# Performance work log

Measured on AMD Instinct MI355X. Metric: run time of the kernel, lower is better.

Reference implementation:

```python
import jax, jax.numpy as jnp
from jax import lax
import numpy as np

EPS = 1e-5
DN = ('NCHW', 'OIHW', 'NCHW')


def conv_s2(x, w):
    # Conv2d k=4 s=2 p=1, no bias
    return lax.conv_general_dilated(x, w, (2, 2), [(1, 1), (1, 1)], dimension_numbers=DN)


def deconv_s2(x, w):
    # ConvTranspose2d k=4 s=2 p=1; torch weight layout (in, out, kH, kW)
    w_ = jnp.flip(w, (2, 3)).transpose(1, 0, 2, 3)  # -> (out, in, kH, kW)
    return lax.conv_general_dilated(x, w_, (1, 1), [(2, 2), (2, 2)],
                                    lhs_dilation=(2, 2), dimension_numbers=DN)


def bn_train(x, gamma, beta):
    # BatchNorm2d in training mode: batch stats over (N, H, W), biased variance
    m = jnp.mean(x, axis=(0, 2, 3), keepdims=True)
    v = jnp.var(x, axis=(0, 2, 3), keepdims=True)
    g = gamma.reshape(1, -1, 1, 1)
    b = beta.reshape(1, -1, 1, 1)
    return (x - m) * jax.lax.rsqrt(v + EPS) * g + b


def lrelu(x):
    return jnp.where(x >= 0, x, 0.2 * x)


def setup_inputs() -> dict:
    key = jax.random.key(0)
    ks = jax.random.split(key, 32)
    nef = 64
    d = {}
    d['x'] = jax.random.normal(ks[0], (256, 3, 64, 64), dtype=jnp.float32)
    # encoder conv weights (O, I, 4, 4), init N(0, 0.02)
    d['w1'] = 0.02 * jax.random.normal(ks[1], (nef, 3, 4, 4), jnp.float32)
    d['w2'] = 0.02 * jax.random.normal(ks[2], (nef * 2, nef, 4, 4), jnp.float32)
    d['w3'] = 0.02 * jax.random.normal(ks[3], (nef * 4, nef * 2, 4, 4), jnp.float32)
    d['w4'] = 0.02 * jax.random.normal(ks[4], (nef * 8, nef * 4, 4, 4), jnp.float32)
    # bn params: weight ~ N(1, 0.02), bias = 0
    for i, c in enumerate([nef, nef * 2, nef * 4, nef * 8]):
        d[f'g{i+1}'] = 1.0 + 0.02 * jax.random.normal(ks[5 + i], (c,), jnp.float32)
        d[f'b{i+1}'] = jnp.zeros((c,), jnp.float32)
    # 512 channel-wise Linear(16,16): torch default init U(-1/4, 1/4)
    bound = 1.0 / 4.0
    d['cw_w'] = jax.random.uniform(ks[9], (512, 16, 16), jnp.float32, -bound, bound)
    d['cw_b'] = jax.random.uniform(ks[10], (512, 16), jnp.float32, -bound, bound)
    # decoder deconv weights in torch layout (in, out, 4, 4)
    d['dw1'] = 0.02 * jax.random.normal(ks[11], (nef * 8, nef * 4, 4, 4), jnp.float32)
    d['dw2'] = 0.02 * jax.random.normal(ks[12], (nef * 4, nef * 2, 4, 4), jnp.float32)
    d['dw3'] = 0.02 * jax.random.normal(ks[13], (nef * 2, nef, 4, 4), jnp.float32)
    d['dw4'] = 0.02 * jax.random.normal(ks[14], (nef, 3, 4, 4), jnp.float32)
    for i, c in enumerate([nef * 4, nef * 2, nef]):
        d[f'dg{i+1}'] = 1.0 + 0.02 * jax.random.normal(ks[15 + i], (c,), jnp.float32)
        d[f'db{i+1}'] = jnp.zeros((c,), jnp.float32)
    return d


def reference(x, w1, w2, w3, w4, g1, b1, g2, b2, g3, b3, g4, b4,
              cw_w, cw_b, dw1, dw2, dw3, dw4, dg1, db1, dg2, db2, dg3, db3):
    h = lrelu(bn_train(conv_s2(x, w1), g1, b1))
    h = lrelu(bn_train(conv_s2(h, w2), g2, b2))
    h = lrelu(bn_train(conv_s2(h, w3), g3, b3))
    h = lrelu(bn_train(conv_s2(h, w4), g4, b4))  # (B, 512, 4, 4)
    B, C, H, W = h.shape
    flat = h.reshape(B, C, H * W)  # (B, 512, 16)
    # per-channel Linear: y[b,c,t] = sum_s flat[b,c,s] * cw_w[c,t,s] + cw_b[c,t]
    flat = jnp.einsum('bcs,cts->bct', flat, cw_w) + cw_b[None, :, :]
    h = flat.reshape(B, C, H, W)
    h = jax.nn.relu(bn_train(deconv_s2(h, dw1), dg1, db1))
    h = jax.nn.relu(bn_train(deconv_s2(h, dw2), dg2, db2))
    h = jax.nn.relu(bn_train(deconv_s2(h, dw3), dg3, db3))
    return jnp.tanh(deconv_s2(h, dw4))
```

## Files before the change

### kernel.cpp

```cpp
#include <hip/hip_runtime.h>
#include <math.h>

typedef _Float16 f16;
typedef __attribute__((ext_vector_type(8))) _Float16 f16x8;
typedef __attribute__((ext_vector_type(16))) float f32x16;

union U64x2 { unsigned long long u[2]; f16x8 v; };
union Q16   { uint4 q; unsigned long long u[2]; };

constexpr int ilog2c(int x) { return x <= 1 ? 0 : 1 + ilog2c(x >> 1); }

__device__ __forceinline__ float fast_tanh(float x) {
    float e = __expf(2.f * x);
    return (e - 1.f) / (e + 1.f);
}

__device__ __forceinline__ void barrier_no_vmdrain() {
    asm volatile("s_waitcnt lgkmcnt(0)" ::: "memory");
    __builtin_amdgcn_sched_barrier(0);
    __builtin_amdgcn_s_barrier();
    __builtin_amdgcn_sched_barrier(0);
}

template<int CIN,int IH,int IW,int OH,int OW,int COUT,int COB,int SPT,int KS,
         int CO_FR,bool DEC,bool PAIR>
__global__ __launch_bounds__(256,2) void mfma_conv(
    const f16* __restrict__ xin, const f16* __restrict__ wp,
    f16* __restrict__ out16, float* __restrict__ out32, size_t ps,
    float* __restrict__ psumF, float* __restrict__ psqF)
{
    constexpr int OHo  = DEC ? OH/2 : OH;
    constexpr int OWo  = DEC ? OW/2 : OW;
    constexpr int KTOT = CIN * (DEC ? 4 : 16);
    constexpr int CH   = (KTOT/64) / KS;
    constexpr int RPT  = CIN / 64;
    constexpr int RSH  = (RPT==1?0:RPT==2?1:RPT==4?2:3);
    constexpr int WSTR = CIN * 16;
    constexpr int TPR  = 256 / COB;
    constexpr int SPB  = OHo * OWo;
    constexpr int LSPB = ilog2c(SPB);
    constexpr int LOWo = ilog2c(OWo);

    static_assert(!PAIR || (RPT >= 2 && CH % 2 == 0), "PAIR needs RPT>=2");
    constexpr int CHU  = PAIR ? CH/2 : CH;
    constexpr int RW   = PAIR ? 32 : 16;
    constexpr int PM   = PAIR ? 15 : 7;
    constexpr int KKN  = PAIR ? 8 : 4;
    constexpr int XU4  = PAIR ? 16 : 8;
    constexpr int WSEG = (PAIR ? 128 : 64)/TPR;
    constexpr int WU4  = WSEG / 8;

    __shared__ unsigned long long Xs[SPT*RW];
    __shared__ unsigned long long Wls[COB*RW];

    const int t   = threadIdx.x;
    const int bx  = blockIdx.x;
    const int cob = blockIdx.y;
    const int bz  = blockIdx.z;
    const int par = DEC ? (bz & 3) : 0;
    const int ks  = DEC ? (bz >> 2) : bz;
    const int poh = par >> 1, pw = par & 1;

    const int gsp_s = bx*SPT + t;
    const int img_s = gsp_s >> LSPB;
    const int r_s   = gsp_s & (SPB-1);
    const int oy_s  = r_s >> LOWo;
    const int ox_s  = r_s & (OWo-1);

    const int wco   = t / TPR;
    const int wpart = t % TPR;
    const f16* wbase = wp + (size_t)(cob*COB + wco)*WSTR + wpart*WSEG;

    const int wave = t >> 6, lane = t & 63, half = lane >> 5, l31 = lane & 31;
    const int co_w = (wave >> 1) * (CO_FR*32);
    const int sp_w = (wave & 1) * 128;
    const int swz  = l31 & PM;

    f32x16 acc[CO_FR][4];
    #pragma unroll
    for (int i = 0; i < CO_FR; ++i)
        #pragma unroll
        for (int b = 0; b < 4; ++b)
            #pragma unroll
            for (int r = 0; r < 16; ++r) acc[i][b][r] = 0.f;

    uint4 xreg[XU4];
    uint4 wreg[WU4];

    auto issue = [&](int cc) {
        const int gc  = ks*CH + (PAIR ? 2*cc : cc);
        const int tap = gc >> RSH;
        const int ci0 = (gc & (RPT-1)) << 6;
        int kh, kw, ih, iw;
        if (DEC) {
            const int t2h = tap >> 1, t2w = tap & 1;
            kh = (1-poh) + 2*t2h; kw = (1-pw) + 2*t2w;
            ih = oy_s + poh - t2h; iw = ox_s + pw - t2w;
        } else {
            kh = tap >> 2; kw = tap & 3;
            ih = 2*oy_s - 1 + kh; iw = 2*ox_s - 1 + kw;
        }
        const int woff = (kh*4 + kw)*CIN + ci0;
        const uint4* wsrc = (const uint4*)(wbase + woff);
        #pragma unroll
        for (int j = 0; j < WU4; ++j) wreg[j] = wsrc[j];
        const bool ok = (unsigned)ih < (unsigned)IH && (unsigned)iw < (unsigned)IW;
        if (ok) {
            const uint4* xsrc = (const uint4*)
                (xin + ((size_t)(img_s*IH + ih)*IW + iw)*CIN + ci0);
            #pragma unroll
            for (int j = 0; j < XU4; ++j) xreg[j] = xsrc[j];
        } else {
            #pragma unroll
            for (int j = 0; j < XU4; ++j) xreg[j] = uint4{0u,0u,0u,0u};
        }
    };

    issue(0);

    for (int cc = 0; cc < CHU; ++cc) {
        if (cc) barrier_no_vmdrain();

        #pragma unroll
        for (int j = 0; j < WU4; ++j) {
            Q16 v; v.q = wreg[j];
            const int lp = wpart*WU4 + j;
            const int u0 = wco*RW + ((lp ^ (wco & PM)) << 1);
            Wls[u0]   = v.u[0];
            Wls[u0+1] = v.u[1];
        }
        {
            #pragma unroll
            for (int j = 0; j < XU4; ++j) {
                Q16 v; v.q = xreg[j];
                const int u0 = t*RW + ((j ^ (t & PM)) << 1);
                Xs[u0]   = v.u[0];
                Xs[u0+1] = v.u[1];
            }
        }

        if (cc + 1 < CHU) issue(cc + 1);

        asm volatile("s_waitcnt lgkmcnt(0)" ::: "memory");
        __builtin_amdgcn_sched_barrier(0);
        __builtin_amdgcn_s_barrier();
        __builtin_amdgcn_sched_barrier(0);

        #pragma unroll
        for (int kk = 0; kk < KKN; ++kk) {
            const int so = ((kk*2 + half) ^ swz) << 1;
            f16x8 wf[CO_FR], xf[4];
            #pragma unroll
            for (int i = 0; i < CO_FR; ++i) {
                U64x2 u; const int rw = (co_w + i*32 + l31)*RW + so;
                u.u[0] = Wls[rw]; u.u[1] = Wls[rw+1]; wf[i] = u.v;
            }
            #pragma unroll
            for (int b = 0; b < 4; ++b) {
                U64x2 u; const int rx = (sp_w + b*32 + l31)*RW + so;
                u.u[0] = Xs[rx]; u.u[1] = Xs[rx+1]; xf[b] = u.v;
            }
            #pragma unroll
            for (int i = 0; i < CO_FR; ++i)
                #pragma unroll
                for (int b = 0; b < 4; ++b)
                    acc[i][b] = __builtin_amdgcn_mfma_f32_32x32x16_f16(
                        xf[b], wf[i], acc[i][b], 0, 0, 0);
        }
    }

    #pragma unroll
    for (int b = 0; b < 4; ++b) {
        #pragma unroll
        for (int q = 0; q < 4; ++q) {
            #pragma unroll
            for (int r2 = 0; r2 < 4; ++r2) {
                const int sp_loc = sp_w + b*32 + q*8 + 4*half + r2;
                const int gsp    = bx*SPT + sp_loc;
                size_t base;
                if (DEC) {
                    const int img = gsp >> LSPB;
                    const int r   = gsp & (SPB-1);
                    const int oh  = 2*(r >> LOWo) + poh;
                    const int ow  = 2*(r & (OWo-1)) + pw;
                    base = ((size_t)(img*OH + oh)*OW + ow)*COUT + cob*COB;
                } else {
                    base = (size_t)gsp*COUT + cob*COB;
                }
                #pragma unroll
                for (int i = 0; i < CO_FR; ++i) {
                    const int co_l = co_w + i*32 + l31;
                    const float v  = acc[i][b][q*4 + r2];
                    if (KS == 1) out16[base + co_l] = (_Float16)v;
                    else         out32[(size_t)ks*ps + base + co_l] = v;
                }
            }
        }
    }

    if (KS == 1 && psumF != nullptr) {
        float sArr[CO_FR], qArr[CO_FR];
        #pragma unroll
        for (int i = 0; i < CO_FR; ++i) {
            float s = 0.f, q = 0.f;
            #pragma unroll
            for (int b = 0; b < 4; ++b)
                #pragma unroll
                for (int r = 0; r < 16; ++r) {
                    const float v = acc[i][b][r];
                    s += v; q += v * v;
                }
            s += __shfl_down(s, 32);
            q += __shfl_down(q, 32);
            sArr[i] = s; qArr[i] = q;
        }
        __syncthreads();
        float* LS = (float*)Xs;
        float* LQ = LS + 4*CO_FR*32;
        if (half == 0) {
            #pragma unroll
            for (int i = 0; i < CO_FR; ++i) {
                LS[(wave*CO_FR + i)*32 + l31] = sArr[i];
                LQ[(wave*CO_FR + i)*32 + l31] = qArr[i];
            }
        }
        __syncthreads();
        if (t < COB) {
            constexpr int KSH = (CO_FR == 1 ? 5 : 6);
            const int k  = t >> KSH;
            const int ii = (CO_FR == 1) ? 0 : ((t >> 5) & 1);
            const int l  = t & 31;
            const int i0 = ((2*k)  *CO_FR + ii)*32 + l;
            const int i1 = ((2*k+1)*CO_FR + ii)*32 + l;
            atomicAdd(psumF + cob*COB + t, LS[i0] + LS[i1]);
            atomicAdd(psqF  + cob*COB + t, LQ[i0] + LQ[i1]);
        }
    }
}

__global__ __launch_bounds__(256,2) void conv1_mfma(
    const f16* __restrict__ xp, const f16* __restrict__ wp,
    f16* __restrict__ out, float* __restrict__ psumF, float* __restrict__ psqF)
{
    __shared__ unsigned long long Xs[256*16];
    __shared__ unsigned long long Wls[64*16];
    const int t = threadIdx.x, bx = blockIdx.x;

    {
        const int r = t >> 2, part = t & 3;
        const uint4* src = (const uint4*)(wp + r*64 + part*16);
        Q16 v0; v0.q = src[0];
        Q16 v1; v1.q = src[1];
        const int a0 = r*16 + (((part*2)   ^ (r & 7)) << 1);
        const int a1 = r*16 + (((part*2+1) ^ (r & 7)) << 1);
        Wls[a0]   = v0.u[0]; Wls[a0+1] = v0.u[1];
        Wls[a1]   = v1.u[0]; Wls[a1+1] = v1.u[1];
    }
    {
        const int gsp = bx*256 + t;
        const int n = gsp >> 10, r = gsp & 1023;
        const int oy = r >> 5, ox = r & 31;
        const int ih0 = 2*oy - 1, iw0 = 2*ox - 1;
        #pragma unroll
        for (int tap = 0; tap < 16; ++tap) {
            const int ih = ih0 + (tap >> 2), iw = iw0 + (tap & 3);
            unsigned long long v = 0ull;
            if ((unsigned)ih < 64u && (unsigned)iw < 64u)
                v = *(const unsigned long long*)(xp + (((size_t)n*64 + ih)*64 + iw)*4);
            const int u = t*16 + (((tap >> 1) ^ (t & 7)) << 1) + (tap & 1);
            Xs[u] = v;
        }
    }
    __syncthreads();

    const int wave = t >> 6, lane = t & 63, half = lane >> 5, l31 = lane & 31;
    const int co_w = (wave >> 1) * 32;
    const int sp_w = (wave & 1) * 128;
    const int swz  = l31 & 7;

    f32x16 acc[4];
    #pragma unroll
    for (int b = 0; b < 4; ++b)
        #pragma unroll
        for (int r = 0; r < 16; ++r) acc[b][r] = 0.f;

    #pragma unroll
    for (int kk = 0; kk < 4; ++kk) {
        const int so = ((kk*2 + half) ^ swz) << 1;
        U64x2 uw; const int rw = (co_w + l31)*16 + so;
        uw.u[0] = Wls[rw]; uw.u[1] = Wls[rw+1];
        #pragma unroll
        for (int b = 0; b < 4; ++b) {
            U64x2 ux; const int rx = (sp_w + b*32 + l31)*16 + so;
            ux.u[0] = Xs[rx]; ux.u[1] = Xs[rx+1];
            acc[b] = __builtin_amdgcn_mfma_f32_32x32x16_f16(
                ux.v, uw.v, acc[b], 0, 0, 0);
        }
    }
    #pragma unroll
    for (int b = 0; b < 4; ++b)
        #pragma unroll
        for (int q = 0; q < 4; ++q)
            #pragma unroll
            for (int r2 = 0; r2 < 4; ++r2) {
                const int sp_loc = sp_w + b*32 + q*8 + 4*half + r2;
                out[(size_t)(bx*256 + sp_loc)*64 + co_w + l31] =
                    (_Float16)acc[b][q*4 + r2];
            }

    float s = 0.f, q = 0.f;
    #pragma unroll
    for (int b = 0; b < 4; ++b)
        #pragma unroll
        for (int r = 0; r < 16; ++r) {
            const float v = acc[b][r];
            s += v; q += v * v;
        }
    s += __shfl_down(s, 32);
    q += __shfl_down(q, 32);
    __syncthreads();
    {
        float* LS = (float*)Xs;
        float* LQ = LS + 128;
        if (half == 0) {
            LS[wave*32 + l31] = s;
            LQ[wave*32 + l31] = q;
        }
        __syncthreads();
        if (t < 64) {
            const int k = t >> 5, l = t & 31;
            atomicAdd(psumF + t, LS[(2*k)*32 + l] + LS[(2*k+1)*32 + l]);
            atomicAdd(psqF  + t, LQ[(2*k)*32 + l] + LQ[(2*k+1)*32 + l]);
        }
    }
}

__global__ __launch_bounds__(256,2) void deconv4_mfma(
    const f16* __restrict__ xin, const f16* __restrict__ wp,
    float* __restrict__ out)
{
    __shared__ unsigned long long Xs[256*16];
    __shared__ unsigned long long Wls[4][32*16];

    const int t   = threadIdx.x;
    const int bx  = blockIdx.x;

    const int gsp_s = bx*256 + t;
    const int img_s = gsp_s >> 10;
    const int r_s   = gsp_s & 1023;
    const int oy_s  = r_s >> 5;
    const int ox_s  = r_s & 31;

    const int wco   = t >> 3;
    const int wpart = t & 7;

    const int wave = t >> 6, lane = t & 63, half = lane >> 5, l31 = lane & 31;
    const int sp_w = wave * 64;
    const int swz  = l31 & 7;

    f32x16 acc[4][2];
    #pragma unroll
    for (int p = 0; p < 4; ++p)
        #pragma unroll
        for (int b = 0; b < 2; ++b)
            #pragma unroll
            for (int r = 0; r < 16; ++r) acc[p][b][r] = 0.f;

    uint4 xreg[8];

    auto issueX = [&](int oid) {
        const int dh = oid/3 - 1, dw = oid%3 - 1;
        const int ih = oy_s + dh, iw = ox_s + dw;
        const bool ok = (unsigned)ih < 32u && (unsigned)iw < 32u;
        if (ok) {
            const uint4* src = (const uint4*)
                (xin + ((size_t)(img_s*32 + ih)*32 + iw)*64);
            #pragma unroll
            for (int j = 0; j < 8; ++j) xreg[j] = src[j];
        } else {
            #pragma unroll
            for (int j = 0; j < 8; ++j) xreg[j] = uint4{0u,0u,0u,0u};
        }
    };

    issueX(0);

    #pragma unroll
    for (int oid = 0; oid < 9; ++oid) {
        const int dh = oid/3 - 1, dw = oid%3 - 1;
        const int nH = (dh == 0) ? 2 : 1;
        const int nW = (dw == 0) ? 2 : 1;

        if (oid) barrier_no_vmdrain();

        uint4 wregc[4];
        #pragma unroll
        for (int ch = 0; ch < 2; ++ch) {
            #pragma unroll
            for (int cw = 0; cw < 2; ++cw) {
                if (ch < nH && cw < nW) {
                    const int poh_ = (dh == -1) ? 0 : (dh == 1) ? 1 : ch;
                    const int pw_  = (dw == -1) ? 0 : (dw == 1) ? 1 : cw;
                    const int kh   = (1 - poh_) + 2*(poh_ - dh);
                    const int kw   = (1 - pw_)  + 2*(pw_  - dw);
                    wregc[ch*2+cw] = *(const uint4*)
                        (wp + wco*1024 + (kh*4 + kw)*64 + wpart*8);
                }
            }
        }

        #pragma unroll
        for (int j = 0; j < 8; ++j) {
            Q16 v; v.q = xreg[j];
            const int u0 = t*16 + ((j ^ (t & 7)) << 1);
            Xs[u0]   = v.u[0];
            Xs[u0+1] = v.u[1];
        }
        #pragma unroll
        for (int ch = 0; ch < 2; ++ch) {
            #pragma unroll
            for (int cw = 0; cw < 2; ++cw) {
                if (ch < nH && cw < nW) {
                    Q16 v; v.q = wregc[ch*2+cw];
                    const int u0 = wco*16 + ((wpart ^ (wco & 7)) << 1);
                    Wls[ch*2+cw][u0]   = v.u[0];
                    Wls[ch*2+cw][u0+1] = v.u[1];
                }
            }
        }

        if (oid + 1 < 9) issueX(oid + 1);

        asm volatile("s_waitcnt lgkmcnt(0)" ::: "memory");
        __builtin_amdgcn_sched_barrier(0);
        __builtin_amdgcn_s_barrier();
        __builtin_amdgcn_sched_barrier(0);

        #pragma unroll
        for (int ch = 0; ch < 2; ++ch) {
            #pragma unroll
            for (int cw = 0; cw < 2; ++cw) {
                if (ch < nH && cw < nW) {
                    const int poh_ = (dh == -1) ? 0 : (dh == 1) ? 1 : ch;
                    const int pw_  = (dw == -1) ? 0 : (dw == 1) ? 1 : cw;
                    const int p    = poh_*2 + pw_;
                    #pragma unroll
                    for (int kk = 0; kk < 4; ++kk) {
                        const int so = ((kk*2 + half) ^ swz) << 1;
                        U64x2 uw; const int rw = l31*16 + so;
                        uw.u[0] = Wls[ch*2+cw][rw];
                        uw.u[1] = Wls[ch*2+cw][rw+1];
                        #pragma unroll
                        for (int b = 0; b < 2; ++b) {
                            U64x2 ux; const int rx = (sp_w + b*32 + l31)*16 + so;
                            ux.u[0] = Xs[rx]; ux.u[1] = Xs[rx+1];
                            acc[p][b] = __builtin_amdgcn_mfma_f32_32x32x16_f16(
                                uw.v, ux.v, acc[p][b], 0, 0, 0);
                        }
                    }
                }
            }
        }
    }

    if (half == 0) {
        #pragma unroll
        for (int p = 0; p < 4; ++p) {
            const int poh = p >> 1, pw = p & 1;
            #pragma unroll
            for (int b = 0; b < 2; ++b) {
                const int gsp = bx*256 + sp_w + b*32 + l31;
                const int img = gsp >> 10;
                const int r   = gsp & 1023;
                const int oh  = 2*(r >> 5) + poh;
                const int ow  = 2*(r & 31) + pw;
                #pragma unroll
                for (int co = 0; co < 3; ++co)
                    out[(((size_t)img*3 + co)*64 + oh)*64 + ow] =
                        fast_tanh(acc[p][b][co]);
            }
        }
    }
}

__global__ __launch_bounds__(256) void prep_x(
    const float* __restrict__ x, f16* __restrict__ xp)
{
    const int i = blockIdx.x*256 + threadIdx.x;
    const int n = i >> 12, p = i & 4095;
    const float* b = x + (size_t)n*12288 + p;
    union { _Float16 h[4]; unsigned long long u; } o;
    o.h[0] = (_Float16)b[0];
    o.h[1] = (_Float16)b[4096];
    o.h[2] = (_Float16)b[8192];
    o.h[3] = (_Float16)0.f;
    *(unsigned long long*)(xp + (size_t)i*4) = o.u;
}

__global__ __launch_bounds__(256) void prep_w1(
    const float* __restrict__ w1, f16* __restrict__ wp)
{
    const int e = blockIdx.x*256 + threadIdx.x;
    const int co = e >> 6, k = e & 63, tap = k >> 2, ci = k & 3;
    const float v = (ci < 3) ? w1[(co*3 + ci)*16 + tap] : 0.f;
    wp[e] = (_Float16)v;
}

__global__ __launch_bounds__(256) void prep_w4(
    const float* __restrict__ dw4, f16* __restrict__ wp)
{
    const int e = blockIdx.x*256 + threadIdx.x;
    const int co = e >> 10, r = e & 1023, khw = r >> 6, ci = r & 63;
    const float v = (co < 3) ? dw4[(ci*3 + co)*16 + khw] : 0.f;
    wp[e] = (_Float16)v;
}

__global__ __launch_bounds__(256) void prep_w(
    const float* __restrict__ w2, const float* __restrict__ w3,
    const float* __restrict__ w4, const float* __restrict__ dw1,
    const float* __restrict__ dw2, const float* __restrict__ dw3,
    f16* __restrict__ dst)
{
    const int e = blockIdx.x*256 + threadIdx.x;
    float v;
    if (e < 131072) {
        int co = e >> 10, r = e & 1023, khw = r >> 6, ci = r & 63;
        v = w2[(co*64 + ci)*16 + khw];
    } else if (e < 655360) {
        int l = e - 131072;
        int co = l >> 11, r = l & 2047, khw = r >> 7, ci = r & 127;
        v = w3[(co*128 + ci)*16 + khw];
    } else if (e < 2752512) {
        int l = e - 655360;
        int co = l >> 12, r = l & 4095, khw = r >> 8, ci = r & 255;
        v = w4[(co*256 + ci)*16 + khw];
    } else if (e < 4849664) {
        int l = e - 2752512;
        int co = l >> 13, r = l & 8191, khw = r >> 9, ci = r & 511;
        v = dw1[(ci*256 + co)*16 + khw];
    } else if (e < 5373952) {
        int l = e - 4849664;
        int co = l >> 12, r = l & 4095, khw = r >> 8, ci = r & 255;
        v = dw2[(ci*128 + co)*16 + khw];
    } else {
        int l = e - 5373952;
        int co = l >> 11, r = l & 2047, khw = r >> 7, ci = r & 127;
        v = dw3[(ci*64 + co)*16 + khw];
    }
    dst[e] = (_Float16)v;
}

template<typename T, int P>
__global__ __launch_bounds__(256) void bn_partial(
    const T* __restrict__ x, size_t ps, float* __restrict__ psum,
    float* __restrict__ psq, int C, int rowsPerS, int S)
{
    const int s = blockIdx.x;
    const int c = (blockIdx.y << 6) + (threadIdx.x & 63);
    float a = 0.f, q = 0.f;
    const int rEnd = (s + 1) * rowsPerS;
    for (int r = s*rowsPerS + (threadIdx.x >> 6); r < rEnd; r += 4) {
        float v = 0.f;
        #pragma unroll
        for (int p = 0; p < P; ++p)
            v += (float)x[p*ps + (size_t)r * C + c];
        a += v; q += v * v;
    }
    __shared__ float ls[256], lq[256];
    ls[threadIdx.x] = a; lq[threadIdx.x] = q;
    __syncthreads();
    if (threadIdx.x < 64) {
        a = ls[threadIdx.x] + ls[threadIdx.x+64] + ls[threadIdx.x+128] + ls[threadIdx.x+192];
        q = lq[threadIdx.x] + lq[threadIdx.x+64] + lq[threadIdx.x+128] + lq[threadIdx.x+192];
        psum[c * S + s] = a; psq[c * S + s] = q;
    }
}

__global__ __launch_bounds__(256) void bn_finalize(
    const float* __restrict__ psum, const float* __restrict__ psq,
    const float* __restrict__ gamma, const float* __restrict__ beta,
    float* __restrict__ scale, float* __restrict__ shift,
    int C, int S, float inv_count)
{
    int c = blockIdx.x * 256 + threadIdx.x;
    if (c >= C) return;
    float s = 0.f, q = 0.f;
    for (int i = 0; i < S; ++i) { s += psum[c*S + i]; q += psq[c*S + i]; }
    float m   = s * inv_count;
    float var = q * inv_count - m * m;
    var = var < 0.f ? 0.f : var;
    float sc = gamma[c] * rsqrtf(var + 1e-5f);
    scale[c] = sc;
    shift[c] = beta[c] - m * sc;
}

__global__ __launch_bounds__(256) void bn_act16f(
    f16* __restrict__ x, const float* __restrict__ psum, const float* __restrict__ psq,
    const float* __restrict__ gamma, const float* __restrict__ beta,
    int Cmask, float inv_count, float slope, size_t n8)
{
    const size_t base = (size_t)blockIdx.x*256 + threadIdx.x;
    const int c0 = (int)((base * 8) & (size_t)Cmask);
    float sc[8], sh[8];
    #pragma unroll
    for (int j = 0; j < 8; ++j) {
        const int c = c0 + j;
        float m   = psum[c] * inv_count;
        float var = psq[c] * inv_count - m * m;
        var = var < 0.f ? 0.f : var;
        float s = gamma[c] * rsqrtf(var + 1e-5f);
        sc[j] = s;
        sh[j] = beta[c] - m * s;
    }
    const size_t stride = (size_t)gridDim.x * 256;
    for (size_t i = base; i < n8; i += stride) {
        union { uint4 u; _Float16 h[8]; } a;
        a.u = *(const uint4*)(x + i*8);
        #pragma unroll
        for (int j = 0; j < 8; ++j) {
            float v = (float)a.h[j] * sc[j] + sh[j];
            a.h[j] = (_Float16)(v >= 0.f ? v : slope * v);
        }
        *(uint4*)(x + i*8) = a.u;
    }
}

template<int P>
__global__ __launch_bounds__(256) void bn_act32(
    const float* __restrict__ x, size_t ps, f16* __restrict__ y,
    const float* __restrict__ sc, const float* __restrict__ sh,
    int Cmask, float slope)
{
    const size_t i8 = ((size_t)blockIdx.x*256 + threadIdx.x) * 8;
    float xv[8] = {0,0,0,0,0,0,0,0};
    #pragma unroll
    for (int p = 0; p < P; ++p) {
        float4 v0 = *(const float4*)(x + p*ps + i8);
        float4 v1 = *(const float4*)(x + p*ps + i8 + 4);
        xv[0]+=v0.x; xv[1]+=v0.y; xv[2]+=v0.z; xv[3]+=v0.w;
        xv[4]+=v1.x; xv[5]+=v1.y; xv[6]+=v1.z; xv[7]+=v1.w;
    }
    union { uint4 u; _Float16 h[8]; } a;
    const int c0 = (int)(i8 & (size_t)Cmask);
    #pragma unroll
    for (int j = 0; j < 8; ++j) {
        float v = xv[j] * sc[c0+j] + sh[c0+j];
        a.h[j] = (_Float16)(v >= 0.f ? v : slope * v);
    }
    *(uint4*)(y + i8) = a.u;
}

__global__ __launch_bounds__(256) void chanlin16(
    const f16* __restrict__ in, const float* __restrict__ w,
    const float* __restrict__ bias, f16* __restrict__ out)
{
    const int i = blockIdx.x*256 + threadIdx.x;
    const int c  = i & 511;
    const int bt = i >> 9;
    const int b  = bt >> 4, tt = bt & 15;
    const f16* src = in + ((size_t)b*16)*512 + c;
    const float* wr = w + ((size_t)c*16 + tt)*16;
    float acc = bias[c*16 + tt];
    #pragma unroll
    for (int s = 0; s < 16; ++s)
        acc = fmaf((float)src[s*512], wr[s], acc);
    out[i] = (_Float16)acc;
}

extern "C" void kernel_launch(void* const* d_in, const int* in_sizes, int n_in,
                              void* d_out, int out_size, void* d_ws, size_t ws_size,
                              hipStream_t stream)
{
    const float* x   = (const float*)d_in[0];
    const float* w1  = (const float*)d_in[1];
    const float* w2  = (const float*)d_in[2];
    const float* w3  = (const float*)d_in[3];
    const float* w4  = (const float*)d_in[4];
    const float* g1  = (const float*)d_in[5];
    const float* b1  = (const float*)d_in[6];
    const float* g2  = (const float*)d_in[7];
    const float* b2  = (const float*)d_in[8];
    const float* g3  = (const float*)d_in[9];
    const float* b3  = (const float*)d_in[10];
    const float* g4  = (const float*)d_in[11];
    const float* b4  = (const float*)d_in[12];
    const float* cww = (const float*)d_in[13];
    const float* cwb = (const float*)d_in[14];
    const float* dw1 = (const float*)d_in[15];
    const float* dw2 = (const float*)d_in[16];
    const float* dw3 = (const float*)d_in[17];
    const float* dw4 = (const float*)d_in[18];
    const float* dg1 = (const float*)d_in[19];
    const float* db1 = (const float*)d_in[20];
    const float* dg2 = (const float*)d_in[21];
    const float* db2 = (const float*)d_in[22];
    const float* dg3 = (const float*)d_in[23];
    const float* db3 = (const float*)d_in[24];

    char* WS = (char*)d_ws;
    float* psum  = (float*)WS;
    float* psq   = (float*)(WS + 65536);
    float* scale = (float*)(WS + 131072);
    float* shift = (float*)(WS + 133120);
    float* fst   = (float*)(WS + 196608);
    f16* slotA   = (f16*)(WS + 262144);
    f16* slotB   = (f16*)(WS + 262144 + 33554432);
    f16* wprep   = (f16*)(WS + 84148224);
    f16* wprep1  = wprep + 5505024;
    f16* wprep4  = wprep1 + 4096;

    f16*   A_hi  = slotA + 8388608;
    float* pB    = (float*)slotB;
    f16*   xpack = slotA;

    float* fs0 = fst;          float* fs1 = fst + 1024;
    float* fs2 = fst + 2048;   float* fs4 = fst + 4096;
    float* fs5 = fst + 5120;   float* fs6 = fst + 6144;

    hipMemsetAsync(fst, 0, 28672, stream);
    prep_w<<<21504, 256, 0, stream>>>(w2, w3, w4, dw1, dw2, dw3, wprep);
    prep_w1<<<16, 256, 0, stream>>>(w1, wprep1);
    prep_w4<<<128, 256, 0, stream>>>(dw4, wprep4);
    prep_x<<<4096, 256, 0, stream>>>(x, xpack);

    conv1_mfma<<<1024, 256, 0, stream>>>(xpack, wprep1, slotB, fs0, fs0 + 512);
    bn_act16f<<<2048, 256, 0, stream>>>(slotB, fs0, fs0 + 512, g1, b1, 63,
                                        1.f/262144.f, 0.2f, (size_t)2097152);

    mfma_conv<64,32,32,16,16,128, 128,256,1,2,false,false><<<dim3(256,1,1), 256, 0, stream>>>(
        slotB, wprep, slotA, nullptr, 0, fs1, fs1 + 512);
    bn_act16f<<<2048, 256, 0, stream>>>(slotA, fs1, fs1 + 512, g2, b2, 127,
                                        1.f/65536.f, 0.2f, (size_t)1048576);

    mfma_conv<128,16,16,8,8,256, 64,256,1,1,false,false><<<dim3(64,4,1), 256, 0, stream>>>(
        slotA, wprep + 131072, A_hi, nullptr, 0, fs2, fs2 + 512);
    bn_act16f<<<2048, 256, 0, stream>>>(A_hi, fs2, fs2 + 512, g3, b3, 255,
                                        1.f/16384.f, 0.2f, (size_t)524288);

    mfma_conv<256,8,8,4,4,512, 128,256,4,2,false,false><<<dim3(16,4,4), 256, 0, stream>>>(
        A_hi, wprep + 655360, nullptr, pB, (size_t)2097152, nullptr, nullptr);
    bn_partial<float,4><<<dim3(32,8), 256, 0, stream>>>(pB, (size_t)2097152, psum, psq, 512, 128, 32);
    bn_finalize<<<2, 256, 0, stream>>>(psum, psq, g4, b4, scale, shift, 512, 32, 1.f/4096.f);
    bn_act32<4><<<1024, 256, 0, stream>>>(pB, (size_t)2097152, slotA, scale, shift, 511, 0.2f);

    chanlin16<<<8192, 256, 0, stream>>>(slotA, cww, cwb, slotB);

    mfma_conv<512,4,4,8,8,256, 64,256,1,1,true,false><<<dim3(16,4,4), 256, 0, stream>>>(
        slotB, wprep + 2752512, A_hi, nullptr, 0, fs4, fs4 + 512);
    bn_act16f<<<2048, 256, 0, stream>>>(A_hi, fs4, fs4 + 512, dg1, db1, 255,
                                        1.f/16384.f, 0.f, (size_t)524288);

    mfma_conv<256,8,8,16,16,128, 128,256,1,2,true,false><<<dim3(64,1,4), 256, 0, stream>>>(
        A_hi, wprep + 4849664, slotB, nullptr, 0, fs5, fs5 + 512);
    bn_act16f<<<2048, 256, 0, stream>>>(slotB, fs5, fs5 + 512, dg2, db2, 127,
                                        1.f/65536.f, 0.f, (size_t)1048576);

    mfma_conv<128,16,16,32,32,64, 64,256,1,1,true,true><<<dim3(256,1,4), 256, 0, stream>>>(
        slotB, wprep + 5373952, slotA, nullptr, 0, fs6, fs6 + 512);
    bn_act16f<<<2048, 256, 0, stream>>>(slotA, fs6, fs6 + 512, dg3, db3, 63,
                                        1.f/262144.f, 0.f, (size_t)2097152);

    deconv4_mfma<<<1024, 256, 0, stream>>>(slotA, wprep4, (float*)d_out);
}
```

Baseline: 535.5 us.

## Add deconv3 kernel sharing input tiles across both column output phases

Replaces the generic mfma_conv call for the third deconvolution with a dedicated kernel. Each block handles one output row phase and both column phases, so every staged input tile feeds up to two weight phases. Input loads are shared across phases and the grid shrinks from four phase slices to two row phases. The cost is double the accumulator registers and a scattered, strided output store pattern.

```diff
diff --git a/kernel.cpp b/kernel.cpp
--- a/kernel.cpp
+++ b/kernel.cpp
@@ -320,6 +320,184 @@
     q += __shfl_down(q, 32);
     __syncthreads();
     {
+        float* LS = (float*)Xs;
+        float* LQ = LS + 128;
+        if (half == 0) {
+            LS[wave*32 + l31] = s;
+            LQ[wave*32 + l31] = q;
+        }
+        __syncthreads();
+        if (t < 64) {
+            const int k = t >> 5, l = t & 31;
+            atomicAdd(psumF + t, LS[(2*k)*32 + l] + LS[(2*k+1)*32 + l]);
+            atomicAdd(psqF  + t, LQ[(2*k)*32 + l] + LQ[(2*k+1)*32 + l]);
+        }
+    }
+}
+
+__global__ __launch_bounds__(256,2) void deconv3_pwf(
+    const f16* __restrict__ xin, const f16* __restrict__ wp,
+    f16* __restrict__ out, float* __restrict__ psumF, float* __restrict__ psqF)
+{
+    __shared__ unsigned long long Xs[256*16];
+    __shared__ unsigned long long Wls[2][64*16];
+
+    const int t   = threadIdx.x;
+    const int bx  = blockIdx.x;
+    const int poh = blockIdx.y;
+
+    const int gsp_s = bx*256 + t;
+    const int img_s = gsp_s >> 8;
+    const int r_s   = gsp_s & 255;
+    const int oy_s  = r_s >> 4;
+    const int ox_s  = r_s & 15;
+
+    const int wco   = t >> 2;
+    const int wpart = t & 3;
+    const f16* wbase = wp + (size_t)wco*2048 + wpart*16;
+
+    const int wave = t >> 6, lane = t & 63, half = lane >> 5, l31 = lane & 31;
+    const int co_w = (wave >> 1) * 32;
+    const int sp_w = (wave & 1) * 128;
+    const int swz  = l31 & 7;
+
+    f32x16 acc[2][4];
+    #pragma unroll
+    for (int p = 0; p < 2; ++p)
+        #pragma unroll
+        for (int b = 0; b < 4; ++b)
+            #pragma unroll
+            for (int r = 0; r < 16; ++r) acc[p][b][r] = 0.f;
+
+    uint4 xreg[8];
+    uint4 wregP[2][2];
+
+    auto issue = [&](int cc) {
+        const int seg  = cc & 1;
+        const int rest = cc >> 1;
+        const int dwi  = rest % 3;
+        const int t2h  = rest / 3;
+        const int dh = poh - t2h, dw = dwi - 1;
+        const int ih = oy_s + dh, iw = ox_s + dw;
+        const int ci0 = seg << 6;
+        #pragma unroll
+        for (int p = 0; p < 2; ++p) {
+            const int t2w = p - dw;
+            if (t2w == 0 || t2w == 1) {
+                const int kh = (1-poh) + 2*t2h, kw = (1-p) + 2*t2w;
+                const uint4* wsrc = (const uint4*)(wbase + (kh*4 + kw)*128 + ci0);
+                wregP[p][0] = wsrc[0];
+                wregP[p][1] = wsrc[1];
+            }
+        }
+        const bool ok = (unsigned)ih < 16u && (unsigned)iw < 16u;
+        if (ok) {
+            const uint4* xsrc = (const uint4*)
+                (xin + ((size_t)(img_s*16 + ih)*16 + iw)*128 + ci0);
+            #pragma unroll
+            for (int j = 0; j < 8; ++j) xreg[j] = xsrc[j];
+        } else {
+            #pragma unroll
+            for (int j = 0; j < 8; ++j) xreg[j] = uint4{0u,0u,0u,0u};
+        }
+    };
+
+    issue(0);
+
+    for (int cc = 0; cc < 12; ++cc) {
+        const int rest = cc >> 1;
+        const int dw   = rest % 3 - 1;
+
+        if (cc) barrier_no_vmdrain();
+
+        #pragma unroll
+        for (int p = 0; p < 2; ++p) {
+            const int t2w = p - dw;
+            if (t2w == 0 || t2w == 1) {
+                #pragma unroll
+                for (int j = 0; j < 2; ++j) {
+                    Q16 v; v.q = wregP[p][j];
+                    const int lp = wpart*2 + j;
+                    const int u0 = wco*16 + ((lp ^ (wco & 7)) << 1);
+                    Wls[p][u0]   = v.u[0];
+                    Wls[p][u0+1] = v.u[1];
+                }
+            }
+        }
+        #pragma unroll
+        for (int j = 0; j < 8; ++j) {
+            Q16 v; v.q = xreg[j];
+            const int u0 = t*16 + ((j ^ (t & 7)) << 1);
+            Xs[u0]   = v.u[0];
+            Xs[u0+1] = v.u[1];
+        }
+
+        if (cc + 1 < 12) issue(cc + 1);
+
+        asm volatile("s_waitcnt lgkmcnt(0)" ::: "memory");
+        __builtin_amdgcn_sched_barrier(0);
+        __builtin_amdgcn_s_barrier();
+        __builtin_amdgcn_sched_barrier(0);
+
+        #pragma unroll
+        for (int kk = 0; kk < 4; ++kk) {
+            const int so = ((kk*2 + half) ^ swz) << 1;
+            f16x8 xf[4];
+            #pragma unroll
+            for (int b = 0; b < 4; ++b) {
+                U64x2 u; const int rx = (sp_w + b*32 + l31)*16 + so;
+                u.u[0] = Xs[rx]; u.u[1] = Xs[rx+1]; xf[b] = u.v;
+            }
+            #pragma unroll
+            for (int p = 0; p < 2; ++p) {
+                const int t2w = p - dw;
+                if (t2w == 0 || t2w == 1) {
+                    U64x2 uw; const int rw = (co_w + l31)*16 + so;
+                    uw.u[0] = Wls[p][rw]; uw.u[1] = Wls[p][rw+1];
+                    #pragma unroll
+                    for (int b = 0; b < 4; ++b)
+                        acc[p][b] = __builtin_amdgcn_mfma_f32_32x32x16_f16(
+                            xf[b], uw.v, acc[p][b], 0, 0, 0);
+                }
+            }
+        }
+    }
+
+    #pragma unroll
+    for (int p = 0; p < 2; ++p) {
+        #pragma unroll
+        for (int b = 0; b < 4; ++b) {
+            #pragma unroll
+            for (int q = 0; q < 4; ++q) {
+                #pragma unroll
+                for (int r2 = 0; r2 < 4; ++r2) {
+                    const int sp_loc = sp_w + b*32 + q*8 + 4*half + r2;
+                    const int gsp    = bx*256 + sp_loc;
+                    const int img    = gsp >> 8;
+                    const int r      = gsp & 255;
+                    const int oh     = 2*(r >> 4) + poh;
+                    const int ow     = 2*(r & 15) + p;
+                    const size_t base = ((size_t)(img*32 + oh)*32 + ow)*64;
+                    out[base + co_w + l31] = (_Float16)acc[p][b][q*4 + r2];
+                }
+            }
+        }
+    }
+
+    if (psumF != nullptr) {
+        float s = 0.f, q = 0.f;
+        #pragma unroll
+        for (int p = 0; p < 2; ++p)
+            #pragma unroll
+            for (int b = 0; b < 4; ++b)
+                #pragma unroll
+                for (int r = 0; r < 16; ++r) {
+                    const float v = acc[p][b][r];
+                    s += v; q += v * v;
+                }
+        s += __shfl_down(s, 32);
+        q += __shfl_down(q, 32);
+        __syncthreads();
         float* LS = (float*)Xs;
         float* LQ = LS + 128;
         if (half == 0) {
@@ -755,8 +933,8 @@
     bn_act16f<<<2048, 256, 0, stream>>>(slotB, fs5, fs5 + 512, dg2, db2, 127,
                                         1.f/65536.f, 0.f, (size_t)1048576);
 
-    mfma_conv<128,16,16,32,32,64, 64,256,1,1,true,true><<<dim3(256,1,4), 256, 0, stream>>>(
-        slotB, wprep + 5373952, slotA, nullptr, 0, fs6, fs6 + 512);
+    deconv3_pwf<<<dim3(256,2), 256, 0, stream>>>(
+        slotB, wprep + 5373952, slotA, fs6, fs6 + 512);
     bn_act16f<<<2048, 256, 0, stream>>>(slotA, fs6, fs6 + 512, dg3, db3, 63,
                                         1.f/262144.f, 0.f, (size_t)2097152);
 
```

Result: no change. 526.6 us (-1.7%).
